# Kernel tuning notes

Measured on AMD Instinct MI355X. Metric: run time of the kernel, lower is better.

Reference implementation:

```python
import jax, jax.numpy as jnp
import numpy as np

N, M, E = 50000, 50000, 1600000
D_IN, HID, OUT = 128, 128, 128


def setup_inputs() -> dict:
    key = jax.random.key(0)
    ks = jax.random.split(key, 8)
    query = jax.random.normal(ks[0], (N, D_IN), jnp.float32)
    memory = jax.random.normal(ks[1], (M, D_IN), jnp.float32)
    adj_vals = jnp.ones((E,), jnp.float32)  # tf.sparse adjacency values (typically 1.0)
    Wq = jax.random.normal(ks[2], (D_IN, HID), jnp.float32) * 0.05
    bq = jnp.zeros((HID,), jnp.float32)
    Wk = jax.random.normal(ks[3], (D_IN, HID), jnp.float32) * 0.05
    bk = jnp.zeros((HID,), jnp.float32)
    Wv = jax.random.normal(ks[4], (D_IN, OUT), jnp.float32) * 0.05
    bv = jnp.zeros((OUT,), jnp.float32)
    rows = jnp.sort(jax.random.randint(ks[5], (E,), 0, N, jnp.int32))
    cols = jax.random.randint(ks[6], (E,), 0, M, jnp.int32)
    return {"query": query, "memory": memory, "adj_vals": adj_vals,
            "Wq": Wq, "bq": bq, "Wk": Wk, "bk": bk, "Wv": Wv, "bv": bv,
            "rows": rows, "cols": cols}


def reference(query, memory, adj_vals, Wq, bq, Wk, bk, Wv, bv, rows, cols):
    n = query.shape[0]
    hid = Wq.shape[1]
    # Dense projections with gelu (tfa.activations.gelu default approximate=True)
    q = jax.nn.gelu(query @ Wq + bq, approximate=True)   # [n, hid]
    k = jax.nn.gelu(memory @ Wk + bk, approximate=True)  # [m, hid]
    v = jax.nn.gelu(memory @ Wv + bv, approximate=True)  # [m, out]
    # Edge-level scores = (q_i . k_j) / sqrt(hid) * adj_val  (== coef * adj_matrix)
    scores = jnp.sum(q[rows] * k[cols], axis=-1)          # [E]
    scores = scores * (adj_vals / jnp.sqrt(jnp.float32(hid)))
    # Sparse softmax over nonzero entries of each row (tf.sparse.softmax)
    row_max = jax.ops.segment_max(scores, rows, num_segments=n, indices_are_sorted=True)
    row_max = jnp.where(jnp.isfinite(row_max), row_max, 0.0)  # rows with no edges
    e = jnp.exp(scores - row_max[rows])
    denom = jax.ops.segment_sum(e, rows, num_segments=n, indices_are_sorted=True)
    w = e / denom[rows]                                   # [E]
    # Sparse-dense matmul: out_i = sum_j w_ij * v_j
    out = jax.ops.segment_sum(w[:, None] * v[cols], rows, num_segments=n, indices_are_sorted=True)
    return out
```

## Files before the change

kernel.cpp:

```cpp
#include <hip/hip_runtime.h>
#include <hip/hip_fp8.h>
#include <math.h>

typedef _Float16 f16x4 __attribute__((ext_vector_type(4)));
typedef _Float16 f16x8 __attribute__((ext_vector_type(8)));
typedef float f32x4 __attribute__((ext_vector_type(4)));
typedef __fp16 hf8 __attribute__((ext_vector_type(8)));

#define DIM 128
#define LDST 136

#if defined(__has_builtin)
#if __has_builtin(__builtin_amdgcn_cvt_pk_fp8_f32) && __has_builtin(__builtin_amdgcn_cvt_pk_f32_fp8)
#define HAVE_FP8CVT 1
#endif
#endif

__device__ __forceinline__ unsigned int pack_fp8x4(float f0, float f1, float f2, float f3) {
#ifdef HAVE_FP8CVT
    int w = __builtin_amdgcn_cvt_pk_fp8_f32(f0, f1, 0, false);
    w = __builtin_amdgcn_cvt_pk_fp8_f32(f2, f3, w, true);
    return (unsigned int)w;
#else
    __hip_fp8_e4m3 a(f0), b(f1), c(f2), d(f3);
    return (unsigned int)a.__x | ((unsigned int)b.__x << 8) |
           ((unsigned int)c.__x << 16) | ((unsigned int)d.__x << 24);
#endif
}

__device__ __forceinline__ void dot_fp8x4(float& d, unsigned int w, const float* qv) {
#ifdef HAVE_FP8CVT
    auto lo = __builtin_amdgcn_cvt_pk_f32_fp8((int)w, false);
    auto hi = __builtin_amdgcn_cvt_pk_f32_fp8((int)w, true);
    d += lo[0] * qv[0] + lo[1] * qv[1] + hi[0] * qv[2] + hi[1] * qv[3];
#else
    for (int j = 0; j < 4; ++j) {
        __hip_fp8_e4m3 t; t.__x = (unsigned char)((w >> (8 * j)) & 0xff);
        d += (float)t * qv[j];
    }
#endif
}

__global__ __launch_bounds__(256) void setup_kernel(
    const float* __restrict__ Wq, const float* __restrict__ Wk,
    const float* __restrict__ Wv, _Float16* __restrict__ Wt,
    const int* __restrict__ rows, int* __restrict__ row_ptr, int n, int e)
{
    int b = blockIdx.x;
    if (b < 192) {
        int mat = b >> 6;
        const float* W = (mat == 0) ? Wq : (mat == 1) ? Wk : Wv;
        _Float16* dst = Wt + (size_t)mat * DIM * DIM;
        int idx = (b & 63) * 256 + threadIdx.x;
        int k = idx >> 7;
        int c = idx & 127;
        dst[c * DIM + k] = (_Float16)W[idx];
    } else {
        int r = (b - 192) * 256 + threadIdx.x;
        if (r > n) return;
        if (r == n) { row_ptr[n] = e; return; }
        int lo = 0, hi = e;
        while (lo < hi) {
            int mid = (lo + hi) >> 1;
            if (rows[mid] < r) lo = mid + 1; else hi = mid;
        }
        row_ptr[r] = lo;
    }
}

__global__ __launch_bounds__(256, 3) void proj_gemm_kernel(
    const float* __restrict__ query, const float* __restrict__ memory,
    const _Float16* __restrict__ Wt,
    const float* __restrict__ bq, const float* __restrict__ bk,
    const float* __restrict__ bv,
    _Float16* __restrict__ qf, unsigned char* __restrict__ k8,
    _Float16* __restrict__ v16, int n, int m)
{
    __shared__ _Float16 xs[128 * LDST];

    int which = blockIdx.y;
    const float* X     = (which == 0) ? query : memory;
    const _Float16* Wm = Wt + (size_t)which * DIM * DIM;
    const float* bias  = (which == 0) ? bq : (which == 1) ? bk : bv;
    int R              = (which == 0) ? n : m;

    int tid = threadIdx.x;
    int rowblock = blockIdx.x * 128;
    if (rowblock >= R) return;

    for (int it = 0; it < 16; ++it) {
        int flat = it * 256 + tid;
        int r  = flat >> 5;
        int c4 = (flat & 31) * 4;
        int gr = rowblock + r;
        if (gr >= R) gr = R - 1;
        float4 x = *(const float4*)(X + (size_t)gr * DIM + c4);
        f16x4 w4;
        w4[0] = (_Float16)x.x; w4[1] = (_Float16)x.y;
        w4[2] = (_Float16)x.z; w4[3] = (_Float16)x.w;
        *(f16x4*)(&xs[r * LDST + c4]) = w4;
    }
    __syncthreads();

    int wave = tid >> 6;
    int lane = tid & 63;
    int quad = lane >> 4;
    int l16  = lane & 15;
    int wrow = wave * 32;

    f16x8 afrag[2][4];
    for (int rt = 0; rt < 2; ++rt)
        for (int ks = 0; ks < 4; ++ks)
            afrag[rt][ks] = *(const f16x8*)(&xs[(wrow + rt * 16 + l16) * LDST + quad * 8 + ks * 32]);

    f32x4 acc[8][2];
    for (int ct = 0; ct < 8; ++ct) { acc[ct][0] = {0,0,0,0}; acc[ct][1] = {0,0,0,0}; }
    for (int ct = 0; ct < 8; ++ct) {
        const _Float16* wp = Wm + (size_t)(ct * 16 + l16) * DIM + quad * 8;
        for (int ks = 0; ks < 4; ++ks) {
            f16x8 b = *(const f16x8*)(wp + ks * 32);
            acc[ct][0] = __builtin_amdgcn_mfma_f32_16x16x32_f16(afrag[0][ks], b, acc[ct][0], 0, 0, 0);
            acc[ct][1] = __builtin_amdgcn_mfma_f32_16x16x32_f16(afrag[1][ks], b, acc[ct][1], 0, 0, 0);
        }
    }

    __syncthreads();
    for (int ct = 0; ct < 8; ++ct) {
        float bval = bias[ct * 16 + l16];
        for (int rt = 0; rt < 2; ++rt) {
            for (int reg = 0; reg < 4; ++reg) {
                float x = acc[ct][rt][reg] + bval;
                float t  = 0.7978845608028654f * (x + 0.044715f * x * x * x);
                float th = 1.0f - 2.0f / (__expf(2.0f * t) + 1.0f);
                float g  = 0.5f * x * (1.0f + th);
                xs[(wrow + rt * 16 + quad * 4 + reg) * LDST + ct * 16 + l16] = (_Float16)g;
            }
        }
    }
    __syncthreads();

    if (which == 1) {
        for (int it = 0; it < 8; ++it) {
            int flat = it * 256 + tid;
            int r  = flat >> 4;
            int c8 = (flat & 15) * 8;
            int gr = rowblock + r;
            if (gr < R) {
                f16x8 h = *(const f16x8*)(&xs[r * LDST + c8]);
                unsigned int w0 = pack_fp8x4((float)h[0], (float)h[1], (float)h[2], (float)h[3]);
                unsigned int w1 = pack_fp8x4((float)h[4], (float)h[5], (float)h[6], (float)h[7]);
                *(uint2*)(k8 + (size_t)gr * DIM + c8) = make_uint2(w0, w1);
            }
        }
    } else {
        _Float16* Ybase = (which == 0) ? qf : v16;
        for (int it = 0; it < 8; ++it) {
            int flat = it * 256 + tid;
            int r  = flat >> 4;
            int c8 = (flat & 15) * 8;
            int gr = rowblock + r;
            if (gr < R) {
                f16x8 vv = *(const f16x8*)(&xs[r * LDST + c8]);
                *(f16x8*)(Ybase + (size_t)gr * DIM + c8) = vv;
            }
        }
    }
}

__global__ __launch_bounds__(256) void edge_attn_kernel(
    const __fp16* __restrict__ qf, const unsigned char* __restrict__ k8,
    const __fp16* __restrict__ v16, const float* __restrict__ adj_vals,
    const int* __restrict__ cols, const int* __restrict__ row_ptr,
    float* __restrict__ out, int n)
{
    int row = blockIdx.x * 4 + (threadIdx.x >> 6);
    if (row >= n) return;
    int lane    = threadIdx.x & 63;
    int quarter = lane >> 4;
    int l16     = lane & 15;

    int start = row_ptr[row];
    int end   = row_ptr[row + 1];

    float qv[8];
    {
        hf8 q8 = *(const hf8*)(qf + (size_t)row * DIM + l16 * 8);
#pragma unroll
        for (int j = 0; j < 8; ++j) qv[j] = (float)q8[j];
    }

    float s_sum = 0.0f;
    float acc[8];
#pragma unroll
    for (int j = 0; j < 8; ++j) acc[j] = 0.0f;

    const float scale = 0.08838834764831845f;

    for (int g = start; g < end; g += 8) {
        int eA = g + quarter;
        int eB = g + 4 + quarter;
        bool vA = eA < end;
        bool vB = eB < end;
        int last = end - 1;
        int iA = vA ? eA : last;
        int iB = vB ? eB : last;
        int   cA = cols[iA];
        int   cB = cols[iB];
        float aA = adj_vals[iA] * scale;
        float aB = adj_vals[iB] * scale;

        uint2 rA = *(const uint2*)(k8 + (size_t)cA * DIM + l16 * 8);
        uint2 rB = *(const uint2*)(k8 + (size_t)cB * DIM + l16 * 8);
        hf8 vA8 = *(const hf8*)(v16 + (size_t)cA * DIM + l16 * 8);
        hf8 vB8 = *(const hf8*)(v16 + (size_t)cB * DIM + l16 * 8);

        float dA = 0.0f, dB = 0.0f;
        dot_fp8x4(dA, rA.x, qv);
        dot_fp8x4(dA, rA.y, qv + 4);
        dot_fp8x4(dB, rB.x, qv);
        dot_fp8x4(dB, rB.y, qv + 4);
        dA += __shfl_xor(dA, 1); dB += __shfl_xor(dB, 1);
        dA += __shfl_xor(dA, 2); dB += __shfl_xor(dB, 2);
        dA += __shfl_xor(dA, 4); dB += __shfl_xor(dB, 4);
        dA += __shfl_xor(dA, 8); dB += __shfl_xor(dB, 8);

        float pA_ = vA ? __expf(dA * aA) : 0.0f;
        float pB_ = vB ? __expf(dB * aB) : 0.0f;
        s_sum += pA_ + pB_;
#pragma unroll
        for (int j = 0; j < 8; ++j)
            acc[j] += pA_ * (float)vA8[j] + pB_ * (float)vB8[j];
    }

    s_sum += __shfl_xor(s_sum, 16);
    s_sum += __shfl_xor(s_sum, 32);
#pragma unroll
    for (int j = 0; j < 8; ++j) {
        acc[j] += __shfl_xor(acc[j], 16);
        acc[j] += __shfl_xor(acc[j], 32);
    }
    float inv = (s_sum > 0.0f) ? 1.0f / s_sum : 0.0f;

    if (quarter == 0) {
        float4* dst = (float4*)(out + (size_t)row * DIM + l16 * 8);
        dst[0] = make_float4(acc[0] * inv, acc[1] * inv, acc[2] * inv, acc[3] * inv);
        dst[1] = make_float4(acc[4] * inv, acc[5] * inv, acc[6] * inv, acc[7] * inv);
    }
}

extern "C" void kernel_launch(void* const* d_in, const int* in_sizes, int n_in,
                              void* d_out, int out_size, void* d_ws, size_t ws_size,
                              hipStream_t stream)
{
    const float* query    = (const float*)d_in[0];
    const float* memory   = (const float*)d_in[1];
    const float* adj_vals = (const float*)d_in[2];
    const float* Wq       = (const float*)d_in[3];
    const float* bq       = (const float*)d_in[4];
    const float* Wk       = (const float*)d_in[5];
    const float* bk       = (const float*)d_in[6];
    const float* Wv       = (const float*)d_in[7];
    const float* bv       = (const float*)d_in[8];
    const int*   rows     = (const int*)d_in[9];
    const int*   cols     = (const int*)d_in[10];
    float* out = (float*)d_out;

    int n = in_sizes[0] / DIM;
    int m = in_sizes[1] / DIM;
    int e = in_sizes[9];

    char* ws = (char*)d_ws;
    size_t off = 0;
    _Float16* Wt  = (_Float16*)(ws + off); off += (size_t)3 * DIM * DIM * 2;
    _Float16* qf  = (_Float16*)(ws + off); off += (size_t)n * DIM * 2;
    _Float16* v16 = (_Float16*)(ws + off); off += (size_t)m * DIM * 2;
    unsigned char* k8 = (unsigned char*)(ws + off); off += (size_t)m * DIM;
    int* row_ptr  = (int*)(ws + off);      off += (size_t)(n + 1) * 4;

    int rp_blocks = (n + 1 + 255) / 256;
    setup_kernel<<<dim3(192 + rp_blocks), 256, 0, stream>>>(
        Wq, Wk, Wv, Wt, rows, row_ptr, n, e);

    proj_gemm_kernel<<<dim3((n + 127) / 128, 3), 256, 0, stream>>>(
        query, memory, Wt, bq, bk, bv, qf, k8, v16, n, m);

    edge_attn_kernel<<<dim3((n + 3) / 4), 256, 0, stream>>>(
        (const __fp16*)qf, k8, (const __fp16*)v16, adj_vals, cols, row_ptr, out, n);
}
```

Baseline: 235.4 us.

## Quantize q, k, v to per-row int8 and use sdot4 for edge scores

The projection kernel now stores q, k and v as int8 with one absmax scale per row, replacing fp16 q/v and fp8 k. The edge kernel uses sdot4 integer dot products and 8 edges per iteration with 16 bytes per lane. This halves the gathered bytes for v and speeds up the score dot product. The cost is larger quantization error, since v moves from fp16 to int8, and an extra scale gather per edge.

After: 221.4 us. 6.0% less time.

```diff
diff --git a/kernel.cpp b/kernel.cpp
--- a/kernel.cpp
+++ b/kernel.cpp
@@ -1,44 +1,34 @@
 #include <hip/hip_runtime.h>
-#include <hip/hip_fp8.h>
 #include <math.h>
 
 typedef _Float16 f16x4 __attribute__((ext_vector_type(4)));
 typedef _Float16 f16x8 __attribute__((ext_vector_type(8)));
 typedef float f32x4 __attribute__((ext_vector_type(4)));
-typedef __fp16 hf8 __attribute__((ext_vector_type(8)));
 
 #define DIM 128
 #define LDST 136
 
 #if defined(__has_builtin)
-#if __has_builtin(__builtin_amdgcn_cvt_pk_fp8_f32) && __has_builtin(__builtin_amdgcn_cvt_pk_f32_fp8)
-#define HAVE_FP8CVT 1
+#if __has_builtin(__builtin_amdgcn_sdot4)
+#define HAVE_SDOT4 1
 #endif
 #endif
 
-__device__ __forceinline__ unsigned int pack_fp8x4(float f0, float f1, float f2, float f3) {
-#ifdef HAVE_FP8CVT
-    int w = __builtin_amdgcn_cvt_pk_fp8_f32(f0, f1, 0, false);
-    w = __builtin_amdgcn_cvt_pk_fp8_f32(f2, f3, w, true);
-    return (unsigned int)w;
+__device__ __forceinline__ int dot4i8(int a, int b, int c) {
+#ifdef HAVE_SDOT4
+    return __builtin_amdgcn_sdot4(a, b, c, false);
 #else
-    __hip_fp8_e4m3 a(f0), b(f1), c(f2), d(f3);
-    return (unsigned int)a.__x | ((unsigned int)b.__x << 8) |
-           ((unsigned int)c.__x << 16) | ((unsigned int)d.__x << 24);
+    int s = c;
+#pragma unroll
+    for (int j = 0; j < 4; ++j)
+        s += (int)((signed char)((a >> (8 * j)) & 0xff)) *
+             (int)((signed char)((b >> (8 * j)) & 0xff));
+    return s;
 #endif
 }
 
-__device__ __forceinline__ void dot_fp8x4(float& d, unsigned int w, const float* qv) {
-#ifdef HAVE_FP8CVT
-    auto lo = __builtin_amdgcn_cvt_pk_f32_fp8((int)w, false);
-    auto hi = __builtin_amdgcn_cvt_pk_f32_fp8((int)w, true);
-    d += lo[0] * qv[0] + lo[1] * qv[1] + hi[0] * qv[2] + hi[1] * qv[3];
-#else
-    for (int j = 0; j < 4; ++j) {
-        __hip_fp8_e4m3 t; t.__x = (unsigned char)((w >> (8 * j)) & 0xff);
-        d += (float)t * qv[j];
-    }
-#endif
+__device__ __forceinline__ float i8f(unsigned int w, int j) {
+    return (float)((signed char)((w >> (8 * j)) & 0xff));
 }
 
 __global__ __launch_bounds__(256) void setup_kernel(
@@ -73,8 +63,9 @@
     const _Float16* __restrict__ Wt,
     const float* __restrict__ bq, const float* __restrict__ bk,
     const float* __restrict__ bv,
-    _Float16* __restrict__ qf, unsigned char* __restrict__ k8,
-    _Float16* __restrict__ v16, int n, int m)
+    unsigned char* __restrict__ q8i, float* __restrict__ sclq,
+    unsigned char* __restrict__ k8i, unsigned char* __restrict__ v8i,
+    float2* __restrict__ scl2, int n, int m)
 {
     __shared__ _Float16 xs[128 * LDST];
 
@@ -139,112 +130,125 @@
     }
     __syncthreads();
 
-    if (which == 1) {
-        for (int it = 0; it < 8; ++it) {
-            int flat = it * 256 + tid;
-            int r  = flat >> 4;
-            int c8 = (flat & 15) * 8;
-            int gr = rowblock + r;
-            if (gr < R) {
-                f16x8 h = *(const f16x8*)(&xs[r * LDST + c8]);
-                unsigned int w0 = pack_fp8x4((float)h[0], (float)h[1], (float)h[2], (float)h[3]);
-                unsigned int w1 = pack_fp8x4((float)h[4], (float)h[5], (float)h[6], (float)h[7]);
-                *(uint2*)(k8 + (size_t)gr * DIM + c8) = make_uint2(w0, w1);
-            }
-        }
-    } else {
-        _Float16* Ybase = (which == 0) ? qf : v16;
-        for (int it = 0; it < 8; ++it) {
-            int flat = it * 256 + tid;
-            int r  = flat >> 4;
-            int c8 = (flat & 15) * 8;
-            int gr = rowblock + r;
-            if (gr < R) {
-                f16x8 vv = *(const f16x8*)(&xs[r * LDST + c8]);
-                *(f16x8*)(Ybase + (size_t)gr * DIM + c8) = vv;
+    unsigned char* Y = (which == 0) ? q8i : (which == 1) ? k8i : v8i;
+    for (int it = 0; it < 8; ++it) {
+        int flat = it * 256 + tid;
+        int r  = flat >> 4;
+        int c8 = (flat & 15) * 8;
+        int gr = rowblock + r;
+        f16x8 h = *(const f16x8*)(&xs[r * LDST + c8]);
+        float f[8];
+        float mx = 0.0f;
+#pragma unroll
+        for (int j = 0; j < 8; ++j) {
+            f[j] = (float)h[j];
+            mx = fmaxf(mx, fabsf(f[j]));
+        }
+        mx = fmaxf(mx, __shfl_xor(mx, 1));
+        mx = fmaxf(mx, __shfl_xor(mx, 2));
+        mx = fmaxf(mx, __shfl_xor(mx, 4));
+        mx = fmaxf(mx, __shfl_xor(mx, 8));
+        float qs = (mx > 0.0f) ? 127.0f / mx : 0.0f;
+        if (gr < R) {
+            unsigned int w0 = 0, w1 = 0;
+#pragma unroll
+            for (int j = 0; j < 4; ++j) {
+                int q = (int)rintf(fminf(fmaxf(f[j] * qs, -127.0f), 127.0f));
+                w0 |= ((unsigned int)(q & 0xff)) << (8 * j);
+            }
+#pragma unroll
+            for (int j = 0; j < 4; ++j) {
+                int q = (int)rintf(fminf(fmaxf(f[4 + j] * qs, -127.0f), 127.0f));
+                w1 |= ((unsigned int)(q & 0xff)) << (8 * j);
+            }
+            *(uint2*)(Y + (size_t)gr * DIM + c8) = make_uint2(w0, w1);
+            if ((flat & 15) == 0) {
+                float ds = mx * (1.0f / 127.0f);
+                if (which == 0)      sclq[gr]   = ds;
+                else if (which == 1) scl2[gr].x = ds;
+                else                 scl2[gr].y = ds;
             }
         }
     }
 }
 
 __global__ __launch_bounds__(256) void edge_attn_kernel(
-    const __fp16* __restrict__ qf, const unsigned char* __restrict__ k8,
-    const __fp16* __restrict__ v16, const float* __restrict__ adj_vals,
+    const unsigned char* __restrict__ q8i, const float* __restrict__ sclq,
+    const unsigned char* __restrict__ k8i, const unsigned char* __restrict__ v8i,
+    const float2* __restrict__ scl2, const float* __restrict__ adj_vals,
     const int* __restrict__ cols, const int* __restrict__ row_ptr,
     float* __restrict__ out, int n)
 {
     int row = blockIdx.x * 4 + (threadIdx.x >> 6);
     if (row >= n) return;
-    int lane    = threadIdx.x & 63;
-    int quarter = lane >> 4;
-    int l16     = lane & 15;
+    int lane = threadIdx.x & 63;
+    int g    = lane >> 3;
+    int d8   = lane & 7;
 
     int start = row_ptr[row];
     int end   = row_ptr[row + 1];
 
-    float qv[8];
-    {
-        hf8 q8 = *(const hf8*)(qf + (size_t)row * DIM + l16 * 8);
-#pragma unroll
-        for (int j = 0; j < 8; ++j) qv[j] = (float)q8[j];
-    }
+    int4  qw = *(const int4*)(q8i + (size_t)row * DIM + d8 * 16);
+    float sq = sclq[row];
 
     float s_sum = 0.0f;
-    float acc[8];
-#pragma unroll
-    for (int j = 0; j < 8; ++j) acc[j] = 0.0f;
+    float acc[16];
+#pragma unroll
+    for (int j = 0; j < 16; ++j) acc[j] = 0.0f;
 
     const float scale = 0.08838834764831845f;
 
-    for (int g = start; g < end; g += 8) {
-        int eA = g + quarter;
-        int eB = g + 4 + quarter;
-        bool vA = eA < end;
-        bool vB = eB < end;
-        int last = end - 1;
-        int iA = vA ? eA : last;
-        int iB = vB ? eB : last;
-        int   cA = cols[iA];
-        int   cB = cols[iB];
-        float aA = adj_vals[iA] * scale;
-        float aB = adj_vals[iB] * scale;
-
-        uint2 rA = *(const uint2*)(k8 + (size_t)cA * DIM + l16 * 8);
-        uint2 rB = *(const uint2*)(k8 + (size_t)cB * DIM + l16 * 8);
-        hf8 vA8 = *(const hf8*)(v16 + (size_t)cA * DIM + l16 * 8);
-        hf8 vB8 = *(const hf8*)(v16 + (size_t)cB * DIM + l16 * 8);
-
-        float dA = 0.0f, dB = 0.0f;
-        dot_fp8x4(dA, rA.x, qv);
-        dot_fp8x4(dA, rA.y, qv + 4);
-        dot_fp8x4(dB, rB.x, qv);
-        dot_fp8x4(dB, rB.y, qv + 4);
-        dA += __shfl_xor(dA, 1); dB += __shfl_xor(dB, 1);
-        dA += __shfl_xor(dA, 2); dB += __shfl_xor(dB, 2);
-        dA += __shfl_xor(dA, 4); dB += __shfl_xor(dB, 4);
-        dA += __shfl_xor(dA, 8); dB += __shfl_xor(dB, 8);
-
-        float pA_ = vA ? __expf(dA * aA) : 0.0f;
-        float pB_ = vB ? __expf(dB * aB) : 0.0f;
-        s_sum += pA_ + pB_;
-#pragma unroll
-        for (int j = 0; j < 8; ++j)
-            acc[j] += pA_ * (float)vA8[j] + pB_ * (float)vB8[j];
-    }
-
+    for (int gg = start; gg < end; gg += 8) {
+        int e     = gg + g;
+        bool vld  = e < end;
+        int  i    = vld ? e : end - 1;
+        int  c    = cols[i];
+        float a   = adj_vals[i] * scale;
+        float2 sk = scl2[c];
+
+        const unsigned char* base = k8i + (size_t)c * DIM + d8 * 16;
+        int4 kw = *(const int4*)base;
+        int4 vw = *(const int4*)(v8i + (size_t)c * DIM + d8 * 16);
+
+        int di = dot4i8(qw.x, kw.x, 0);
+        di = dot4i8(qw.y, kw.y, di);
+        di = dot4i8(qw.z, kw.z, di);
+        di = dot4i8(qw.w, kw.w, di);
+        di += __shfl_xor(di, 1);
+        di += __shfl_xor(di, 2);
+        di += __shfl_xor(di, 4);
+
+        float score = (float)di * (sq * sk.x) * a;
+        float p = vld ? __expf(score) : 0.0f;
+        s_sum += p;
+
+        float psv = p * sk.y;
+#pragma unroll
+        for (int j = 0; j < 4; ++j) {
+            acc[j]      += psv * i8f((unsigned int)vw.x, j);
+            acc[4 + j]  += psv * i8f((unsigned int)vw.y, j);
+            acc[8 + j]  += psv * i8f((unsigned int)vw.z, j);
+            acc[12 + j] += psv * i8f((unsigned int)vw.w, j);
+        }
+    }
+
+    s_sum += __shfl_xor(s_sum, 8);
     s_sum += __shfl_xor(s_sum, 16);
     s_sum += __shfl_xor(s_sum, 32);
 #pragma unroll
-    for (int j = 0; j < 8; ++j) {
+    for (int j = 0; j < 16; ++j) {
+        acc[j] += __shfl_xor(acc[j], 8);
         acc[j] += __shfl_xor(acc[j], 16);
         acc[j] += __shfl_xor(acc[j], 32);
     }
     float inv = (s_sum > 0.0f) ? 1.0f / s_sum : 0.0f;
 
-    if (quarter == 0) {
-        float4* dst = (float4*)(out + (size_t)row * DIM + l16 * 8);
-        dst[0] = make_float4(acc[0] * inv, acc[1] * inv, acc[2] * inv, acc[3] * inv);
-        dst[1] = make_float4(acc[4] * inv, acc[5] * inv, acc[6] * inv, acc[7] * inv);
+    if (g == 0) {
+        float4* dst = (float4*)(out + (size_t)row * DIM + d8 * 16);
+#pragma unroll
+        for (int j = 0; j < 4; ++j)
+            dst[j] = make_float4(acc[4 * j] * inv, acc[4 * j + 1] * inv,
+                                 acc[4 * j + 2] * inv, acc[4 * j + 3] * inv);
     }
 }
 
@@ -271,19 +275,21 @@
 
     char* ws = (char*)d_ws;
     size_t off = 0;
-    _Float16* Wt  = (_Float16*)(ws + off); off += (size_t)3 * DIM * DIM * 2;
-    _Float16* qf  = (_Float16*)(ws + off); off += (size_t)n * DIM * 2;
-    _Float16* v16 = (_Float16*)(ws + off); off += (size_t)m * DIM * 2;
-    unsigned char* k8 = (unsigned char*)(ws + off); off += (size_t)m * DIM;
-    int* row_ptr  = (int*)(ws + off);      off += (size_t)(n + 1) * 4;
+    _Float16* Wt = (_Float16*)(ws + off);       off += (size_t)3 * DIM * DIM * 2;
+    unsigned char* q8i = (unsigned char*)(ws + off); off += (size_t)n * DIM;
+    unsigned char* k8i = (unsigned char*)(ws + off); off += (size_t)m * DIM;
+    unsigned char* v8i = (unsigned char*)(ws + off); off += (size_t)m * DIM;
+    float* sclq  = (float*)(ws + off);          off += (size_t)n * 4;
+    float2* scl2 = (float2*)(ws + off);         off += (size_t)m * 8;
+    int* row_ptr = (int*)(ws + off);            off += (size_t)(n + 1) * 4;
 
     int rp_blocks = (n + 1 + 255) / 256;
     setup_kernel<<<dim3(192 + rp_blocks), 256, 0, stream>>>(
         Wq, Wk, Wv, Wt, rows, row_ptr, n, e);
 
     proj_gemm_kernel<<<dim3((n + 127) / 128, 3), 256, 0, stream>>>(
-        query, memory, Wt, bq, bk, bv, qf, k8, v16, n, m);
+        query, memory, Wt, bq, bk, bv, q8i, sclq, k8i, v8i, scl2, n, m);
 
     edge_attn_kernel<<<dim3((n + 3) / 4), 256, 0, stream>>>(
-        (const __fp16*)qf, k8, (const __fp16*)v16, adj_vals, cols, row_ptr, out, n);
-}
+        q8i, sclq, k8i, v8i, scl2, adj_vals, cols, row_ptr, out, n);
+}
```
